# Optimization experiments

Hardware: AMD Instinct MI355X
Metric: run time of the kernel (lower is better)

## Reference

```python
import jax, jax.numpy as jnp
import numpy as np

SIGMA = 0.1  # kernel-point influence radius (KPConv linear correlation)


def setup_inputs() -> dict:
    key = jax.random.key(0)
    k1, k2, k3, k4, k5 = jax.random.split(key, 5)
    N, K, KP, CIN, COUT = 65536, 32, 15, 64, 128
    pos = jax.random.uniform(k1, (N, 3), dtype=jnp.float32)
    feats = jax.random.normal(k2, (N, CIN), dtype=jnp.float32)
    kernel_points = jax.random.normal(k3, (KP, 3), dtype=jnp.float32) * 0.05
    weights = jax.random.normal(k4, (KP, CIN, COUT), dtype=jnp.float32) / np.sqrt(KP * CIN)
    neighbors = jax.random.randint(k5, (N, K), 0, N, dtype=jnp.int64)
    return {"pos": pos, "feats": feats, "kernel_points": kernel_points,
            "weights": weights, "neighbors": neighbors}


def reference(pos, feats, kernel_points, weights, neighbors):
    # pos: [N,3], feats: [N,Cin], kernel_points: [Kp,3],
    # weights: [Kp,Cin,Cout], neighbors: [N,K] int
    neigh_pos = pos[neighbors]                      # [N,K,3] irregular gather
    rel = neigh_pos - pos[:, None, :]               # [N,K,3]
    # distance from each relative neighbor offset to each kernel point
    d = rel[:, :, None, :] - kernel_points[None, None, :, :]   # [N,K,Kp,3]
    dist = jnp.sqrt(jnp.sum(d * d, axis=-1))        # [N,K,Kp]
    infl = jnp.maximum(0.0, 1.0 - dist / SIGMA)     # linear correlation
    neigh_feat = feats[neighbors]                   # [N,K,Cin] irregular gather
    # per-kernel-point weighted neighbor aggregation, then projection
    weighted = jnp.einsum('njk,njc->nkc', infl, neigh_feat)    # [N,Kp,Cin]
    out = jnp.einsum('nkc,kcd->nd', weighted, weights)         # [N,Cout]
    return out
```

## Files before the change

kernel.cpp:

```cpp
#include <hip/hip_runtime.h>

#define NPTS  65536
#define KNB   32
#define KPn   15
#define CIN   64
#define COUT  128
#define MPTS  32
#define THREADS 1024
#define WSTRIDE 968
#define NTILE 8
#define KSTEPS 30
#define WELEMS (NTILE * KSTEPS * 64 * 8)

typedef __attribute__((ext_vector_type(8))) short short8;
typedef __attribute__((ext_vector_type(4))) float f32x4;

__device__ __forceinline__ unsigned int f2bf(float f) {
    union { float f; unsigned int i; } v; v.f = f;
    return (v.i + 0x7fffu + ((v.i >> 16) & 1u)) >> 16;
}

__global__ void wtrans_kernel(const float* __restrict__ w,
                              const float* __restrict__ kpts,
                              unsigned short* __restrict__ wTf,
                              float4* __restrict__ kpq_out) {
    const int d = blockIdx.x * 256 + threadIdx.x;
    if (d < WELEMS) {
        const int j    = d & 7;
        const int lane = (d >> 3) & 63;
        const int ks   = (d >> 9) % KSTEPS;
        const int t    = d / (KSTEPS * 512);
        const int f    = ks * 32 + (lane >> 4) * 8 + j;
        const int cg   = f / 120;
        const int rem  = f - cg * 120;
        const int orig = (rem >> 3) * 64 + cg * 8 + (rem & 7);
        const int n    = t * 16 + (lane & 15);
        wTf[d] = (unsigned short)f2bf(w[(size_t)orig * COUT + n]);
    }
    if (blockIdx.x == 0 && threadIdx.x < 16) {
        const int k = threadIdx.x;
        if (k < KPn) {
            const float x = kpts[k * 3 + 0];
            const float y = kpts[k * 3 + 1];
            const float z = kpts[k * 3 + 2];
            kpq_out[k] = make_float4(x, y, z, x * x + y * y + z * z);
        } else {
            float mx = 0.f;
            for (int i = 0; i < KPn; ++i) {
                const float x = kpts[i * 3 + 0];
                const float y = kpts[i * 3 + 1];
                const float z = kpts[i * 3 + 2];
                mx = fmaxf(mx, x * x + y * y + z * z);
            }
            const float R = 0.1f + sqrtf(mx);
            kpq_out[15] = make_float4(R * R, 0.f, 0.f, 0.f);
        }
    }
}

#define ACC_HALF(MHALF, BASE, ACCV)                                           \
    {                                                                         \
        unsigned long long mh_ = (MHALF);                                     \
        while (mh_) {                                                         \
            const int j_ = (int)__builtin_ctzll(mh_) + (BASE);                \
            mh_ &= mh_ - 1;                                                   \
            const int nb_ = __builtin_amdgcn_readlane(nbv, j_);               \
            const unsigned int wp_ =                                          \
                (unsigned int)__builtin_amdgcn_readlane((int)wpk[k >> 1], j_);\
            const float w_ = (float)((wp_ >> (16 * (k & 1))) & 0xFFFFu) *     \
                             (1.0f / 65535.0f);                               \
            ACCV += w_ * feats[(size_t)nb_ * CIN + lane];                     \
        }                                                                     \
    }

__global__ __launch_bounds__(THREADS, 8) void kpconv_kernel(
    const float* __restrict__ pos,
    const float* __restrict__ feats,
    const unsigned short* __restrict__ wTf,
    const float4* __restrict__ kpq_in,
    const int*   __restrict__ neighbors,
    float*       __restrict__ out)
{
    __shared__ __align__(16) unsigned short wl[MPTS * WSTRIDE];

    const int tid  = threadIdx.x;
    const int n0   = blockIdx.x * MPTS;
    const int lane = tid & 63;
    const int wv   = tid >> 6;
    const int m    = lane & 15;
    const int q    = lane >> 4;

    const int nbv = neighbors[(size_t)n0 * KNB + tid];
    const float px = pos[(size_t)nbv * 3 + 0];
    const float py = pos[(size_t)nbv * 3 + 1];
    const float pz = pos[(size_t)nbv * 3 + 2];

    const int nAu = __builtin_amdgcn_readfirstlane(n0 + wv * 2);
    const float cxA = pos[(size_t)nAu * 3 + 0];
    const float cyA = pos[(size_t)nAu * 3 + 1];
    const float czA = pos[(size_t)nAu * 3 + 2];
    const float cxB = pos[(size_t)(nAu + 1) * 3 + 0];
    const float cyB = pos[(size_t)(nAu + 1) * 3 + 1];
    const float czB = pos[(size_t)(nAu + 1) * 3 + 2];

    const bool isA = (lane < 32);
    const float rx = px - (isA ? cxA : cxB);
    const float ry = py - (isA ? cyA : cyB);
    const float rz = pz - (isA ? czA : czB);
    const float d2r = rx * rx + ry * ry + rz * rz;

    unsigned int kmask = 0;
    unsigned int wpk[8] = {0u, 0u, 0u, 0u, 0u, 0u, 0u, 0u};
    #pragma unroll
    for (int k = 0; k < KPn; ++k) {
        const float4 kp  = kpq_in[k];
        const float  dot = rx * kp.x + ry * kp.y + rz * kp.z;
        if (dot > 0.5f * (d2r - 0.01f + kp.w)) {
            const float dd = fmaxf(d2r - 2.f * dot + kp.w, 0.f);
            const float w  = 1.0f - 10.0f * sqrtf(dd);
            const unsigned int w16 = (unsigned int)(w * 65535.0f + 0.5f);
            wpk[k >> 1] |= w16 << (16 * (k & 1));
            kmask |= 1u << k;
        }
    }

    {
        const int cg = lane >> 3, j8 = lane & 7;
        unsigned short* const wpA = wl + (wv * 2 + 0) * WSTRIDE + cg * 120 + j8;
        unsigned short* const wpB = wl + (wv * 2 + 1) * WSTRIDE + cg * 120 + j8;
        #pragma unroll
        for (int k = 0; k < KPn; ++k) {
            const unsigned long long mk = __ballot((kmask >> k) & 1u);
            float aA = 0.f, aB = 0.f;
            ACC_HALF(mk & 0x00000000ffffffffull, 0, aA);
            ACC_HALF(mk >> 32, 32, aB);
            wpA[k * 8] = (unsigned short)f2bf(aA);
            wpB[k * 8] = (unsigned short)f2bf(aB);
        }
    }
    __syncthreads();

    {
        const int mt = wv >> 3;
        const int nt = wv & 7;

        f32x4 o0 = {0.f, 0.f, 0.f, 0.f};
        f32x4 o1 = {0.f, 0.f, 0.f, 0.f};
        const unsigned short* ap = wl + (mt * 16 + m) * WSTRIDE + q * 8;
        const short8* bp = (const short8*)wTf + (size_t)nt * KSTEPS * 64 + lane;

        #pragma unroll 3
        for (int ks = 0; ks < KSTEPS; ks += 2) {
            const short8 a0 = *(const short8*)(ap + ks * 32);
            const short8 b0 = bp[ks * 64];
            o0 = __builtin_amdgcn_mfma_f32_16x16x32_bf16(a0, b0, o0, 0, 0, 0);
            const short8 a1 = *(const short8*)(ap + (ks + 1) * 32);
            const short8 b1 = bp[(ks + 1) * 64];
            o1 = __builtin_amdgcn_mfma_f32_16x16x32_bf16(a1, b1, o1, 0, 0, 0);
        }
        o0 = o0 + o1;

        const int c = nt * 16 + m;
        #pragma unroll
        for (int r = 0; r < 4; ++r)
            out[(size_t)(n0 + mt * 16 + q * 4 + r) * COUT + c] = o0[r];
    }
}

extern "C" void kernel_launch(void* const* d_in, const int* in_sizes, int n_in,
                              void* d_out, int out_size, void* d_ws, size_t ws_size,
                              hipStream_t stream) {
    const float* pos       = (const float*)d_in[0];
    const float* feats     = (const float*)d_in[1];
    const float* kpts      = (const float*)d_in[2];
    const float* weights   = (const float*)d_in[3];
    const int*   neighbors = (const int*)d_in[4];
    float*       out       = (float*)d_out;
    unsigned short* wTf    = (unsigned short*)d_ws;
    float4* kpq            = (float4*)((char*)d_ws + WELEMS * 2);

    wtrans_kernel<<<(WELEMS + 255) / 256, 256, 0, stream>>>(weights, kpts, wTf, kpq);
    kpconv_kernel<<<NPTS / MPTS, THREADS, 0, stream>>>(
        pos, feats, wTf, kpq, neighbors, out);
}
```

Before: 142.6 us.

## Halve block threads and give each wave two point rows per weight tile

The block size drops from 1024 to 512 threads. Each wave now runs the neighbor gather/aggregation phase twice, once for each half of the 32-point tile. In the MFMA phase each wave computes both 16-row tiles for one output column tile, so every loaded B (weight) fragment is reused across two MFMAs. This halves global weight-fragment loads per block and cuts the number of waves, in exchange for longer serial gather work per wave and lower thread-level parallelism for latency hiding.

After: 140.4 us. About the same (-1.5%).

```diff
diff --git a/kernel.cpp b/kernel.cpp
--- a/kernel.cpp
+++ b/kernel.cpp
@@ -6,7 +6,7 @@
 #define CIN   64
 #define COUT  128
 #define MPTS  32
-#define THREADS 1024
+#define THREADS 512
 #define WSTRIDE 968
 #define NTILE 8
 #define KSTEPS 30
@@ -90,80 +90,95 @@
     const int m    = lane & 15;
     const int q    = lane >> 4;
 
-    const int nbv = neighbors[(size_t)n0 * KNB + tid];
-    const float px = pos[(size_t)nbv * 3 + 0];
-    const float py = pos[(size_t)nbv * 3 + 1];
-    const float pz = pos[(size_t)nbv * 3 + 2];
-
-    const int nAu = __builtin_amdgcn_readfirstlane(n0 + wv * 2);
-    const float cxA = pos[(size_t)nAu * 3 + 0];
-    const float cyA = pos[(size_t)nAu * 3 + 1];
-    const float czA = pos[(size_t)nAu * 3 + 2];
-    const float cxB = pos[(size_t)(nAu + 1) * 3 + 0];
-    const float cyB = pos[(size_t)(nAu + 1) * 3 + 1];
-    const float czB = pos[(size_t)(nAu + 1) * 3 + 2];
-
-    const bool isA = (lane < 32);
-    const float rx = px - (isA ? cxA : cxB);
-    const float ry = py - (isA ? cyA : cyB);
-    const float rz = pz - (isA ? czA : czB);
-    const float d2r = rx * rx + ry * ry + rz * rz;
-
-    unsigned int kmask = 0;
-    unsigned int wpk[8] = {0u, 0u, 0u, 0u, 0u, 0u, 0u, 0u};
     #pragma unroll
-    for (int k = 0; k < KPn; ++k) {
-        const float4 kp  = kpq_in[k];
-        const float  dot = rx * kp.x + ry * kp.y + rz * kp.z;
-        if (dot > 0.5f * (d2r - 0.01f + kp.w)) {
-            const float dd = fmaxf(d2r - 2.f * dot + kp.w, 0.f);
-            const float w  = 1.0f - 10.0f * sqrtf(dd);
-            const unsigned int w16 = (unsigned int)(w * 65535.0f + 0.5f);
-            wpk[k >> 1] |= w16 << (16 * (k & 1));
-            kmask |= 1u << k;
-        }
-    }
-
-    {
-        const int cg = lane >> 3, j8 = lane & 7;
-        unsigned short* const wpA = wl + (wv * 2 + 0) * WSTRIDE + cg * 120 + j8;
-        unsigned short* const wpB = wl + (wv * 2 + 1) * WSTRIDE + cg * 120 + j8;
+    for (int it = 0; it < 2; ++it) {
+        const int pb = n0 + it * 16;
+
+        const int nbv = neighbors[(size_t)pb * KNB + tid];
+        const float px = pos[(size_t)nbv * 3 + 0];
+        const float py = pos[(size_t)nbv * 3 + 1];
+        const float pz = pos[(size_t)nbv * 3 + 2];
+
+        const int nAu = __builtin_amdgcn_readfirstlane(pb + wv * 2);
+        const float cxA = pos[(size_t)nAu * 3 + 0];
+        const float cyA = pos[(size_t)nAu * 3 + 1];
+        const float czA = pos[(size_t)nAu * 3 + 2];
+        const float cxB = pos[(size_t)(nAu + 1) * 3 + 0];
+        const float cyB = pos[(size_t)(nAu + 1) * 3 + 1];
+        const float czB = pos[(size_t)(nAu + 1) * 3 + 2];
+
+        const bool isA = (lane < 32);
+        const float rx = px - (isA ? cxA : cxB);
+        const float ry = py - (isA ? cyA : cyB);
+        const float rz = pz - (isA ? czA : czB);
+        const float d2r = rx * rx + ry * ry + rz * rz;
+
+        unsigned int kmask = 0;
+        unsigned int wpk[8] = {0u, 0u, 0u, 0u, 0u, 0u, 0u, 0u};
         #pragma unroll
         for (int k = 0; k < KPn; ++k) {
-            const unsigned long long mk = __ballot((kmask >> k) & 1u);
-            float aA = 0.f, aB = 0.f;
-            ACC_HALF(mk & 0x00000000ffffffffull, 0, aA);
-            ACC_HALF(mk >> 32, 32, aB);
-            wpA[k * 8] = (unsigned short)f2bf(aA);
-            wpB[k * 8] = (unsigned short)f2bf(aB);
+            const float4 kp  = kpq_in[k];
+            const float  dot = rx * kp.x + ry * kp.y + rz * kp.z;
+            if (dot > 0.5f * (d2r - 0.01f + kp.w)) {
+                const float dd = fmaxf(d2r - 2.f * dot + kp.w, 0.f);
+                const float w  = 1.0f - 10.0f * sqrtf(dd);
+                const unsigned int w16 = (unsigned int)(w * 65535.0f + 0.5f);
+                wpk[k >> 1] |= w16 << (16 * (k & 1));
+                kmask |= 1u << k;
+            }
+        }
+
+        {
+            const int cg = lane >> 3, j8 = lane & 7;
+            const int rowA = it * 16 + wv * 2;
+            unsigned short* const wpA = wl + (rowA + 0) * WSTRIDE + cg * 120 + j8;
+            unsigned short* const wpB = wl + (rowA + 1) * WSTRIDE + cg * 120 + j8;
+            #pragma unroll
+            for (int k = 0; k < KPn; ++k) {
+                const unsigned long long mk = __ballot((kmask >> k) & 1u);
+                float aA = 0.f, aB = 0.f;
+                ACC_HALF(mk & 0x00000000ffffffffull, 0, aA);
+                ACC_HALF(mk >> 32, 32, aB);
+                wpA[k * 8] = (unsigned short)f2bf(aA);
+                wpB[k * 8] = (unsigned short)f2bf(aB);
+            }
         }
     }
     __syncthreads();
 
     {
-        const int mt = wv >> 3;
-        const int nt = wv & 7;
-
-        f32x4 o0 = {0.f, 0.f, 0.f, 0.f};
-        f32x4 o1 = {0.f, 0.f, 0.f, 0.f};
-        const unsigned short* ap = wl + (mt * 16 + m) * WSTRIDE + q * 8;
+        const int nt = wv;
+        f32x4 o00 = {0.f, 0.f, 0.f, 0.f};
+        f32x4 o01 = {0.f, 0.f, 0.f, 0.f};
+        f32x4 o10 = {0.f, 0.f, 0.f, 0.f};
+        f32x4 o11 = {0.f, 0.f, 0.f, 0.f};
+        const unsigned short* ap0 = wl + m * WSTRIDE + q * 8;
+        const unsigned short* ap1 = wl + (16 + m) * WSTRIDE + q * 8;
         const short8* bp = (const short8*)wTf + (size_t)nt * KSTEPS * 64 + lane;
 
         #pragma unroll 3
         for (int ks = 0; ks < KSTEPS; ks += 2) {
-            const short8 a0 = *(const short8*)(ap + ks * 32);
-            const short8 b0 = bp[ks * 64];
-            o0 = __builtin_amdgcn_mfma_f32_16x16x32_bf16(a0, b0, o0, 0, 0, 0);
-            const short8 a1 = *(const short8*)(ap + (ks + 1) * 32);
-            const short8 b1 = bp[(ks + 1) * 64];
-            o1 = __builtin_amdgcn_mfma_f32_16x16x32_bf16(a1, b1, o1, 0, 0, 0);
-        }
-        o0 = o0 + o1;
+            const short8 b0  = bp[ks * 64];
+            const short8 b1  = bp[(ks + 1) * 64];
+            const short8 a00 = *(const short8*)(ap0 + ks * 32);
+            const short8 a01 = *(const short8*)(ap0 + (ks + 1) * 32);
+            const short8 a10 = *(const short8*)(ap1 + ks * 32);
+            const short8 a11 = *(const short8*)(ap1 + (ks + 1) * 32);
+            o00 = __builtin_amdgcn_mfma_f32_16x16x32_bf16(a00, b0, o00, 0, 0, 0);
+            o10 = __builtin_amdgcn_mfma_f32_16x16x32_bf16(a10, b0, o10, 0, 0, 0);
+            o01 = __builtin_amdgcn_mfma_f32_16x16x32_bf16(a01, b1, o01, 0, 0, 0);
+            o11 = __builtin_amdgcn_mfma_f32_16x16x32_bf16(a11, b1, o11, 0, 0, 0);
+        }
+        o00 = o00 + o01;
+        o10 = o10 + o11;
 
         const int c = nt * 16 + m;
         #pragma unroll
         for (int r = 0; r < 4; ++r)
-            out[(size_t)(n0 + mt * 16 + q * 4 + r) * COUT + c] = o0[r];
+            out[(size_t)(n0 + q * 4 + r) * COUT + c] = o00[r];
+        #pragma unroll
+        for (int r = 0; r < 4; ++r)
+            out[(size_t)(n0 + 16 + q * 4 + r) * COUT + c] = o10[r];
     }
 }
 
```
